# Performance work log

Hardware: AMD Instinct MI355X
Metric: run time of the kernel (lower is better)

## Reference

```python
import jax, jax.numpy as jnp
import numpy as np
from jax import lax

SCALE = 128.0        # x/y/w/h scale = model input size
MIN_SCORE = 0.5      # min_score_thresh
IOU_THRESH = 0.3     # mediapipe min_suppression_threshold
MAX_DET = 64         # fixed detection slots (jit-safe replacement for dynamic list)
NUM_ANCHORS = 896


def _decode(raw_boxes, anchors):
    # raw_boxes [B,A,16], anchors [A,4] = (x_center, y_center, w, h)
    ax, ay, aw, ah = anchors[:, 0], anchors[:, 1], anchors[:, 2], anchors[:, 3]
    xc = raw_boxes[..., 0] / SCALE * aw + ax
    yc = raw_boxes[..., 1] / SCALE * ah + ay
    w = raw_boxes[..., 2] / SCALE * aw
    h = raw_boxes[..., 3] / SCALE * ah
    box = jnp.stack([yc - h / 2, xc - w / 2, yc + h / 2, xc + w / 2], axis=-1)  # [B,A,4] ymin,xmin,ymax,xmax
    kp = raw_boxes[..., 4:16].reshape(*raw_boxes.shape[:-1], 6, 2)  # [B,A,6,2] (x,y)
    kpx = kp[..., 0] / SCALE * aw[:, None] + ax[:, None]
    kpy = kp[..., 1] / SCALE * ah[:, None] + ay[:, None]
    kps = jnp.stack([kpx, kpy], axis=-1).reshape(*raw_boxes.shape[:-1], 12)
    return jnp.concatenate([box, kps], axis=-1)  # [B,A,16]


def _iou(box, boxes):
    # box [4], boxes [A,4]; coords = ymin,xmin,ymax,xmax
    ymin = jnp.maximum(box[0], boxes[:, 0])
    xmin = jnp.maximum(box[1], boxes[:, 1])
    ymax = jnp.minimum(box[2], boxes[:, 2])
    xmax = jnp.minimum(box[3], boxes[:, 3])
    inter = jnp.maximum(ymax - ymin, 0.0) * jnp.maximum(xmax - xmin, 0.0)
    a1 = jnp.maximum(box[2] - box[0], 0.0) * jnp.maximum(box[3] - box[1], 0.0)
    a2 = jnp.maximum(boxes[:, 2] - boxes[:, 0], 0.0) * jnp.maximum(boxes[:, 3] - boxes[:, 1], 0.0)
    return inter / jnp.maximum(a1 + a2 - inter, 1e-6)


def _weighted_nms_single(coords, scores):
    # coords [A,16], scores [A] -> out [MAX_DET,17] sorted by descending score, zero-padded
    rem = jnp.where(scores >= MIN_SCORE, scores, -1.0)

    def step(rem, _):
        idx = jnp.argmax(rem)
        best = rem[idx]
        iou = _iou(coords[idx, :4], coords[:, :4])
        overlap = (iou > IOU_THRESH) & (rem > 0.0)
        wts = jnp.where(overlap, scores, 0.0)            # weight = candidate score
        denom = jnp.maximum(wts.sum(), 1e-6)
        blended = (coords * wts[:, None]).sum(0) / denom  # weighted box + keypoints
        det = jnp.concatenate([blended, best[None]])
        det = jnp.where(best > 0.0, det, jnp.zeros(17, det.dtype))
        rem = jnp.where(overlap, -1.0, rem)
        return rem, det

    _, out = lax.scan(step, rem, None, length=MAX_DET)
    return out


def _project(dets, matrix):
    # dets [B,MAX_DET,17], matrix [B,8] (first two rows of row-major 4x4 affine)
    m = matrix[:, None, :]  # [B,1,8]
    x_idx = jnp.array([1, 3, 4, 6, 8, 10, 12, 14])
    y_idx = jnp.array([0, 2, 5, 7, 9, 11, 13, 15])
    xs = dets[..., x_idx]
    ys = dets[..., y_idx]
    new_x = xs * m[..., 0:1] + ys * m[..., 1:2] + m[..., 3:4]
    new_y = xs * m[..., 4:5] + ys * m[..., 5:6] + m[..., 7:8]
    out = dets.at[..., x_idx].set(new_x)
    out = out.at[..., y_idx].set(new_y)
    # keep padded (invalid) rows zero, like the segmented-tensor original
    valid = dets[..., 16:17] > 0.0
    return jnp.where(valid, out, 0.0)


def _rescale(dets, h, w):
    hf = jnp.float32(h)
    wf = jnp.float32(w)
    scale = jnp.concatenate([
        jnp.array([1.0, 1.0]) * 0 + jnp.stack([hf, wf]),   # ymin*h, xmin*w
        jnp.stack([hf, wf]),                               # ymax*h, xmax*w
        jnp.tile(jnp.stack([wf, hf]), 6),                  # kp x*w, kp y*h
        jnp.ones((1,), jnp.float32),                       # score unchanged
    ])
    return dets * scale


def setup_inputs() -> dict:
    key = jax.random.key(0)
    k1, k2, k3, k4 = jax.random.split(key, 4)
    B = 2048
    return {
        "raw_boxes": jax.random.normal(k1, (B, NUM_ANCHORS, 16), jnp.float32),
        "raw_scores": jax.random.normal(k2, (B, NUM_ANCHORS), jnp.float32),
        "anchors": jax.random.uniform(k3, (NUM_ANCHORS, 4), jnp.float32),
        "transform_matrix": jax.random.normal(k4, (B, 8), jnp.float32),
        "h": 720,
        "w": 1280,
    }


def reference(raw_boxes, raw_scores, anchors, transform_matrix, h, w):
    coords = _decode(raw_boxes, anchors)                       # [B,A,16]
    scores = jax.nn.sigmoid(jnp.clip(raw_scores, -100.0, 100.0))
    dets = jax.vmap(_weighted_nms_single)(coords, scores)      # [B,MAX_DET,17]
    dets = _project(dets, transform_matrix)
    dets = _rescale(dets, h, w)
    return dets
```

## Files before the change

### kernel.cpp

```cpp
#include <hip/hip_runtime.h>
#include <math.h>

#define NANCH 896
#define MAXD 64
#define NS 14

__global__ __launch_bounds__(256, 2) void blaze_wave_kernel(
    const float* __restrict__ raw_boxes,
    const float* __restrict__ raw_scores,
    const float* __restrict__ anchors,
    const float* __restrict__ tmat,
    const int* __restrict__ hptr,
    const int* __restrict__ wptr,
    float* __restrict__ out,
    int B)
{
    __shared__ float4 sbox[4][NANCH];
    __shared__ float  sdet[4][17];

    const int lane = threadIdx.x & 63;
    const int wv   = threadIdx.x >> 6;
    const int b    = blockIdx.x * 4 + wv;
    if (b >= B) return;

    const float* rb = raw_boxes  + (size_t)b * (NANCH * 16);
    const float* rs = raw_scores + (size_t)b * NANCH;
    const float inv = 1.f / 128.f;

    const float* M = tmat + (size_t)b * 8;
    const float m0 = M[0], m1 = M[1], m3 = M[3];
    const float m4 = M[4], m5 = M[5], m7 = M[7];
    const float hf = (float)(*hptr);
    const float wf = (float)(*wptr);

    float xv[NS];
#pragma unroll
    for (int j = 0; j < NS; ++j) xv[j] = rs[lane + 64 * j];

    bool  act[NS];
    float4 r0v[NS], anv[NS];
#pragma unroll
    for (int j = 0; j < NS; ++j) {
        act[j] = (xv[j] >= 0.f);
        const int a2 = act[j] ? (lane + 64 * j) : 0;
        r0v[j] = *(const float4*)(rb + a2 * 16);
        anv[j] = *(const float4*)(anchors + a2 * 4);
    }

    float rem[NS];
#pragma unroll
    for (int j = 0; j < NS; ++j) {
        float x = fminf(fmaxf(xv[j], -100.f), 100.f);
        float s = 1.f / (1.f + expf(-x));
        rem[j] = act[j] ? s : -1.f;
    }

    float b0[NS], b1[NS], b2[NS], b3[NS], ar[NS];
#pragma unroll
    for (int j = 0; j < NS; ++j) {
        float xc = r0v[j].x * inv * anv[j].z + anv[j].x;
        float yc = r0v[j].y * inv * anv[j].w + anv[j].y;
        float ww = r0v[j].z * inv * anv[j].z;
        float hh = r0v[j].w * inv * anv[j].w;
        b0[j] = yc - hh * 0.5f; b1[j] = xc - ww * 0.5f;
        b2[j] = yc + hh * 0.5f; b3[j] = xc + ww * 0.5f;
        ar[j] = fmaxf(b2[j] - b0[j], 0.f) * fmaxf(b3[j] - b1[j], 0.f);
        sbox[wv][lane + 64 * j] = make_float4(b0[j], b1[j], b2[j], b3[j]);
    }

    float* ob = out + (size_t)b * (MAXD * 17);
    const bool isx = (lane < 16) && ((0x555Au >> lane) & 1u);

    int iter = 0;
    while (true) {
        float bv = -2.f; int bi = 1 << 30;
#pragma unroll
        for (int j = 0; j < NS; ++j) {
            if (rem[j] > bv) { bv = rem[j]; bi = lane + 64 * j; }
        }
#pragma unroll
        for (int s2 = 32; s2 >= 1; s2 >>= 1) {
            float ov = __shfl_xor(bv, s2, 64);
            int   oi = __shfl_xor(bi, s2, 64);
            if (ov > bv || (ov == bv && oi < bi)) { bv = ov; bi = oi; }
        }

        if (bv <= 0.f) {
            int n = (MAXD - iter) * 17;
            float* op = ob + iter * 17;
            for (int e = lane; e < n; e += 64) op[e] = 0.f;
            break;
        }

        float4 bb = sbox[wv][bi];
        const float bby0 = bb.x, bbx0 = bb.y, bby1 = bb.z, bbx1 = bb.w;
        const float a1 = fmaxf(bby1 - bby0, 0.f) * fmaxf(bbx1 - bbx0, 0.f);

        float acc[16];
#pragma unroll
        for (int c = 0; c < 16; ++c) acc[c] = 0.f;
        float wsum = 0.f;
        bool anyov = false;

#pragma unroll
        for (int j = 0; j < NS; ++j) {
            float yA = fmaxf(bby0, b0[j]);
            float xA = fmaxf(bbx0, b1[j]);
            float yB = fminf(bby1, b2[j]);
            float xB = fminf(bbx1, b3[j]);
            float inter = fmaxf(yB - yA, 0.f) * fmaxf(xB - xA, 0.f);
            if (inter > 0.f) {
                float iou = inter / fmaxf(a1 + ar[j] - inter, 1e-6f);
                if (iou > 0.3f && rem[j] > 0.f) {
                    anyov = true;
                    float wj = rem[j];
                    rem[j] = -1.f;
                    wsum += wj;
                    acc[0] += b0[j] * wj; acc[1] += b1[j] * wj;
                    acc[2] += b2[j] * wj; acc[3] += b3[j] * wj;
                    const int a = lane + 64 * j;
                    float4 an = *(const float4*)(anchors + a * 4);
                    const float* rp = rb + a * 16;
                    float4 r1 = *(const float4*)(rp + 4);
                    float4 r2 = *(const float4*)(rp + 8);
                    float4 r3 = *(const float4*)(rp + 12);
                    acc[4]  += (r1.x * inv * an.z + an.x) * wj;
                    acc[5]  += (r1.y * inv * an.w + an.y) * wj;
                    acc[6]  += (r1.z * inv * an.z + an.x) * wj;
                    acc[7]  += (r1.w * inv * an.w + an.y) * wj;
                    acc[8]  += (r2.x * inv * an.z + an.x) * wj;
                    acc[9]  += (r2.y * inv * an.w + an.y) * wj;
                    acc[10] += (r2.z * inv * an.z + an.x) * wj;
                    acc[11] += (r2.w * inv * an.w + an.y) * wj;
                    acc[12] += (r3.x * inv * an.z + an.x) * wj;
                    acc[13] += (r3.y * inv * an.w + an.y) * wj;
                    acc[14] += (r3.z * inv * an.z + an.x) * wj;
                    acc[15] += (r3.w * inv * an.w + an.y) * wj;
                }
            }
        }

        const unsigned long long mm = __ballot(anyov);
        const bool stuck = (mm == 0ull);

        float tot[16]; float ws;
        if (stuck) {
#pragma unroll
            for (int c = 0; c < 16; ++c) tot[c] = 0.f;
            ws = 0.f;
        } else if (__popcll(mm) == 1) {
            const int src = (int)__ffsll((long long)mm) - 1;
#pragma unroll
            for (int c = 0; c < 16; ++c) tot[c] = __shfl(acc[c], src, 64);
            ws = __shfl(wsum, src, 64);
        } else {
#pragma unroll
            for (int s2 = 32; s2 >= 1; s2 >>= 1) {
                wsum += __shfl_xor(wsum, s2, 64);
#pragma unroll
                for (int c = 0; c < 16; ++c) acc[c] += __shfl_xor(acc[c], s2, 64);
            }
#pragma unroll
            for (int c = 0; c < 16; ++c) tot[c] = acc[c];
            ws = wsum;
        }

        float q = tot[0];
#pragma unroll
        for (int k = 1; k < 16; ++k) q = (lane == k) ? tot[k] : q;
        const float dnm = fmaxf(ws, 1e-6f);
        q = q / dnm;
        const float p = __shfl(q, lane ^ 1, 64);
        float detc;
        if (lane >= 16) detc = bv;
        else detc = isx ? (q * m0 + p * m1 + m3) * wf
                        : (p * m4 + q * m5 + m7) * hf;

        if (stuck) {
            if (lane < 17) sdet[wv][lane] = detc;
            int n = (MAXD - iter) * 17;
            float* op = ob + iter * 17;
            int c = lane % 17;
            for (int e = lane; e < n; e += 64) {
                op[e] = sdet[wv][c];
                c += 13; if (c >= 17) c -= 17;
            }
            break;
        } else {
            if (lane < 17) ob[iter * 17 + lane] = detc;
            ++iter;
            if (iter == MAXD) break;
        }
    }
}

extern "C" void kernel_launch(void* const* d_in, const int* in_sizes, int n_in,
                              void* d_out, int out_size, void* d_ws, size_t ws_size,
                              hipStream_t stream) {
    (void)n_in; (void)out_size; (void)d_ws; (void)ws_size;
    const float* raw_boxes  = (const float*)d_in[0];
    const float* raw_scores = (const float*)d_in[1];
    const float* anchors    = (const float*)d_in[2];
    const float* tmat       = (const float*)d_in[3];
    const int*   hptr       = (const int*)d_in[4];
    const int*   wptr       = (const int*)d_in[5];
    float* out = (float*)d_out;

    const int B = in_sizes[0] / (NANCH * 16);
    blaze_wave_kernel<<<(B + 3) / 4, 256, 0, stream>>>(raw_boxes, raw_scores, anchors,
                                                       tmat, hptr, wptr, out, B);
}
```

Baseline: 184.5 us.

## Compact active anchors into dense slots and launch one wave per block

Result: slower. 189.6 us (+2.8%).

```diff
diff --git a/kernel.cpp b/kernel.cpp
--- a/kernel.cpp
+++ b/kernel.cpp
@@ -5,7 +5,7 @@
 #define MAXD 64
 #define NS 14
 
-__global__ __launch_bounds__(256, 2) void blaze_wave_kernel(
+__global__ __launch_bounds__(64, 2) void blaze_wave_kernel(
     const float* __restrict__ raw_boxes,
     const float* __restrict__ raw_scores,
     const float* __restrict__ anchors,
@@ -15,12 +15,13 @@
     float* __restrict__ out,
     int B)
 {
-    __shared__ float4 sbox[4][NANCH];
-    __shared__ float  sdet[4][17];
-
-    const int lane = threadIdx.x & 63;
-    const int wv   = threadIdx.x >> 6;
-    const int b    = blockIdx.x * 4 + wv;
+    __shared__ float4 cbox[NANCH];
+    __shared__ float  cscore[NANCH];
+    __shared__ unsigned short cidx[NANCH];
+    __shared__ float  sdet[17];
+
+    const int lane = threadIdx.x;
+    const int b    = blockIdx.x;
     if (b >= B) return;
 
     const float* rb = raw_boxes  + (size_t)b * (NANCH * 16);
@@ -47,25 +48,50 @@
         anv[j] = *(const float4*)(anchors + a2 * 4);
     }
 
-    float rem[NS];
+    float sv[NS];
 #pragma unroll
     for (int j = 0; j < NS; ++j) {
         float x = fminf(fmaxf(xv[j], -100.f), 100.f);
-        float s = 1.f / (1.f + expf(-x));
-        rem[j] = act[j] ? s : -1.f;
-    }
-
-    float b0[NS], b1[NS], b2[NS], b3[NS], ar[NS];
+        sv[j] = 1.f / (1.f + expf(-x));
+    }
+
+    int base = 0;
 #pragma unroll
     for (int j = 0; j < NS; ++j) {
         float xc = r0v[j].x * inv * anv[j].z + anv[j].x;
         float yc = r0v[j].y * inv * anv[j].w + anv[j].y;
         float ww = r0v[j].z * inv * anv[j].z;
         float hh = r0v[j].w * inv * anv[j].w;
-        b0[j] = yc - hh * 0.5f; b1[j] = xc - ww * 0.5f;
-        b2[j] = yc + hh * 0.5f; b3[j] = xc + ww * 0.5f;
-        ar[j] = fmaxf(b2[j] - b0[j], 0.f) * fmaxf(b3[j] - b1[j], 0.f);
-        sbox[wv][lane + 64 * j] = make_float4(b0[j], b1[j], b2[j], b3[j]);
+        float y0 = yc - hh * 0.5f, x0 = xc - ww * 0.5f;
+        float y1 = yc + hh * 0.5f, x1 = xc + ww * 0.5f;
+        unsigned long long m = __ballot(act[j]);
+        int pos = base + __popcll(m & ((1ull << lane) - 1ull));
+        if (act[j]) {
+            cbox[pos]   = make_float4(y0, x0, y1, x1);
+            cscore[pos] = sv[j];
+            cidx[pos]   = (unsigned short)(lane + 64 * j);
+        }
+        base += __popcll(m);
+    }
+    const int nact = base;
+    const int nsc  = (nact + 63) >> 6;
+
+    float cb0[NS], cb1[NS], cb2[NS], cb3[NS], car[NS], rem[NS];
+    int   corig[NS];
+#pragma unroll
+    for (int k = 0; k < NS; ++k) {
+        rem[k] = -1.f;
+        if (k < nsc) {
+            int p = k * 64 + lane;
+            bool v = (p < nact);
+            int pc = v ? p : 0;
+            float4 bb = cbox[pc];
+            float sc  = cscore[pc];
+            corig[k]  = (int)cidx[pc];
+            cb0[k] = bb.x; cb1[k] = bb.y; cb2[k] = bb.z; cb3[k] = bb.w;
+            car[k] = fmaxf(bb.z - bb.x, 0.f) * fmaxf(bb.w - bb.y, 0.f);
+            if (v) rem[k] = sc;
+        }
     }
 
     float* ob = out + (size_t)b * (MAXD * 17);
@@ -75,8 +101,8 @@
     while (true) {
         float bv = -2.f; int bi = 1 << 30;
 #pragma unroll
-        for (int j = 0; j < NS; ++j) {
-            if (rem[j] > bv) { bv = rem[j]; bi = lane + 64 * j; }
+        for (int j = 0; j < NS; ++j) if (j < nsc) {
+            if (rem[j] > bv) { bv = rem[j]; bi = j * 64 + lane; }
         }
 #pragma unroll
         for (int s2 = 32; s2 >= 1; s2 >>= 1) {
@@ -92,7 +118,7 @@
             break;
         }
 
-        float4 bb = sbox[wv][bi];
+        float4 bb = cbox[bi];
         const float bby0 = bb.x, bbx0 = bb.y, bby1 = bb.z, bbx1 = bb.w;
         const float a1 = fmaxf(bby1 - bby0, 0.f) * fmaxf(bbx1 - bbx0, 0.f);
 
@@ -103,24 +129,24 @@
         bool anyov = false;
 
 #pragma unroll
-        for (int j = 0; j < NS; ++j) {
-            float yA = fmaxf(bby0, b0[j]);
-            float xA = fmaxf(bbx0, b1[j]);
-            float yB = fminf(bby1, b2[j]);
-            float xB = fminf(bbx1, b3[j]);
+        for (int j = 0; j < NS; ++j) if (j < nsc) {
+            float yA = fmaxf(bby0, cb0[j]);
+            float xA = fmaxf(bbx0, cb1[j]);
+            float yB = fminf(bby1, cb2[j]);
+            float xB = fminf(bbx1, cb3[j]);
             float inter = fmaxf(yB - yA, 0.f) * fmaxf(xB - xA, 0.f);
             if (inter > 0.f) {
-                float iou = inter / fmaxf(a1 + ar[j] - inter, 1e-6f);
+                float iou = inter / fmaxf(a1 + car[j] - inter, 1e-6f);
                 if (iou > 0.3f && rem[j] > 0.f) {
                     anyov = true;
                     float wj = rem[j];
                     rem[j] = -1.f;
                     wsum += wj;
-                    acc[0] += b0[j] * wj; acc[1] += b1[j] * wj;
-                    acc[2] += b2[j] * wj; acc[3] += b3[j] * wj;
-                    const int a = lane + 64 * j;
-                    float4 an = *(const float4*)(anchors + a * 4);
-                    const float* rp = rb + a * 16;
+                    acc[0] += cb0[j] * wj; acc[1] += cb1[j] * wj;
+                    acc[2] += cb2[j] * wj; acc[3] += cb3[j] * wj;
+                    const int orig = corig[j];
+                    float4 an = *(const float4*)(anchors + orig * 4);
+                    const float* rp = rb + orig * 16;
                     float4 r1 = *(const float4*)(rp + 4);
                     float4 r2 = *(const float4*)(rp + 8);
                     float4 r3 = *(const float4*)(rp + 12);
@@ -143,16 +169,19 @@
         const unsigned long long mm = __ballot(anyov);
         const bool stuck = (mm == 0ull);
 
-        float tot[16]; float ws;
+        float q, dnm;
         if (stuck) {
-#pragma unroll
-            for (int c = 0; c < 16; ++c) tot[c] = 0.f;
-            ws = 0.f;
+            q = 0.f; dnm = 1e-6f;
         } else if (__popcll(mm) == 1) {
             const int src = (int)__ffsll((long long)mm) - 1;
-#pragma unroll
-            for (int c = 0; c < 16; ++c) tot[c] = __shfl(acc[c], src, 64);
-            ws = __shfl(wsum, src, 64);
+            float t = __shfl(acc[0], src, 64);
+#pragma unroll
+            for (int c = 1; c < 16; ++c) {
+                float tc = __shfl(acc[c], src, 64);
+                t = (lane == c) ? tc : t;
+            }
+            q   = t;
+            dnm = fmaxf(__shfl(wsum, src, 64), 1e-6f);
         } else {
 #pragma unroll
             for (int s2 = 32; s2 >= 1; s2 >>= 1) {
@@ -160,29 +189,25 @@
 #pragma unroll
                 for (int c = 0; c < 16; ++c) acc[c] += __shfl_xor(acc[c], s2, 64);
             }
-#pragma unroll
-            for (int c = 0; c < 16; ++c) tot[c] = acc[c];
-            ws = wsum;
-        }
-
-        float q = tot[0];
-#pragma unroll
-        for (int k = 1; k < 16; ++k) q = (lane == k) ? tot[k] : q;
-        const float dnm = fmaxf(ws, 1e-6f);
+            float t = acc[0];
+#pragma unroll
+            for (int c2 = 1; c2 < 16; ++c2) t = (lane == c2) ? acc[c2] : t;
+            q = t; dnm = fmaxf(wsum, 1e-6f);
+        }
+
         q = q / dnm;
         const float p = __shfl(q, lane ^ 1, 64);
-        float detc;
-        if (lane >= 16) detc = bv;
-        else detc = isx ? (q * m0 + p * m1 + m3) * wf
-                        : (p * m4 + q * m5 + m7) * hf;
+        const float detc = (lane >= 16) ? bv
+                         : (isx ? (q * m0 + p * m1 + m3) * wf
+                                : (p * m4 + q * m5 + m7) * hf);
 
         if (stuck) {
-            if (lane < 17) sdet[wv][lane] = detc;
+            if (lane < 17) sdet[lane] = detc;
             int n = (MAXD - iter) * 17;
             float* op = ob + iter * 17;
             int c = lane % 17;
             for (int e = lane; e < n; e += 64) {
-                op[e] = sdet[wv][c];
+                op[e] = sdet[c];
                 c += 13; if (c >= 17) c -= 17;
             }
             break;
@@ -207,6 +232,6 @@
     float* out = (float*)d_out;
 
     const int B = in_sizes[0] / (NANCH * 16);
-    blaze_wave_kernel<<<(B + 3) / 4, 256, 0, stream>>>(raw_boxes, raw_scores, anchors,
-                                                       tmat, hptr, wptr, out, B);
+    blaze_wave_kernel<<<B, 64, 0, stream>>>(raw_boxes, raw_scores, anchors,
+                                            tmat, hptr, wptr, out, B);
 }
```
